# Kernel optimization log

Hardware: AMD Instinct MI355X
Metric: run time of the kernel (lower is better)

Reference implementation:

```python
import jax, jax.numpy as jnp
import numpy as np

N_SLOTS = 16
AGG_THRESHOLD = 0.5
EPS_NORM = 1e-12   # torch F.normalize eps
EPS_AGG = 1e-8


def _l2_normalize(x, axis=-1):
    n = jnp.linalg.norm(x, axis=axis, keepdims=True)
    return x / jnp.maximum(n, EPS_NORM)


def setup_inputs() -> dict:
    key = jax.random.key(0)
    B, N, D = 64, 1024, 768
    features = jax.random.normal(key, (B, N, D), dtype=jnp.float32)
    return {"features": features, "batch_size": B}


def reference(features, batch_size):
    # Greedy slot initialization, saliency_mode='norm', aggregate=True.
    B, N, D = features.shape
    features_norm = _l2_normalize(features, axis=-1)          # [B,N,D]
    saliency = jnp.linalg.norm(features, axis=-1)             # [B,N]

    def step(mask, _):
        # mask: [B,N] multiplicative suppression state
        masked_saliency = saliency * mask
        idx = jnp.argmax(masked_saliency, axis=-1)            # [B]
        selected = jnp.take_along_axis(
            features, idx[:, None, None], axis=1)[:, 0]       # [B,D]
        selected_norm = _l2_normalize(selected, axis=-1)      # [B,D]
        similarity = jnp.einsum('bnd,bd->bn', features_norm, selected_norm)
        # aggregate=True path
        agg_w = jnp.clip(similarity * mask, 0.0, None)
        agg_w = agg_w * (similarity > AGG_THRESHOLD).astype(features.dtype)
        agg_w = agg_w / (jnp.sum(agg_w, axis=-1, keepdims=True) + EPS_AGG)
        slot = jnp.einsum('bn,bnd->bd', agg_w, features)      # [B,D]
        new_mask = mask * (1.0 - jnp.clip(similarity, 0.0, 1.0))
        return new_mask, slot

    init_mask = jnp.ones((B, N), dtype=features.dtype)
    _, slots = jax.lax.scan(step, init_mask, None, length=N_SLOTS)
    return jnp.transpose(slots, (1, 0, 2))                    # [B, n_slots, D]
```

## Files before the change

kernel.cpp:

```cpp
#include <hip/hip_runtime.h>
#include <hip/hip_fp16.h>
#include <math.h>

#define B_      64
#define N_      1024
#define D_      768
#define T_      16
#define SLABS   32
#define ROWS_PB 32
#define ROWS_PW 8
#define THR     256
#define CPL     24
#define NTILE   36
#define WFG     8
#define WFTHR   192

typedef _Float16 half8 __attribute__((ext_vector_type(8)));
typedef float    f32x4 __attribute__((ext_vector_type(4)));

__device__ __forceinline__ float wave_sum(float v) {
    #pragma unroll
    for (int off = 32; off; off >>= 1) v += __shfl_xor(v, off);
    return v;
}
__device__ __forceinline__ float half_sum(float v) {
    #pragma unroll
    for (int off = 16; off; off >>= 1) v += __shfl_xor(v, off);
    return v;
}
__device__ __forceinline__ unsigned pack2(float a, float b) {
    __half2 h = __float22half2_rn(make_float2(a, b));
    return *(unsigned*)&h;
}
__device__ __forceinline__ void unpack8(uint4 u, float* f) {
    __half2 h; float2 q;
    h = *(__half2*)&u.x; q = __half22float2(h); f[0] = q.x; f[1] = q.y;
    h = *(__half2*)&u.y; q = __half22float2(h); f[2] = q.x; f[3] = q.y;
    h = *(__half2*)&u.z; q = __half22float2(h); f[4] = q.x; f[5] = q.y;
    h = *(__half2*)&u.w; q = __half22float2(h); f[6] = q.x; f[7] = q.y;
}

__device__ __forceinline__ void gload_lds16(const void* g, void* l) {
    __builtin_amdgcn_global_load_lds(
        (__attribute__((address_space(1))) void*)(g),
        (__attribute__((address_space(3))) void*)(l), 16, 0, 0);
}

__global__ __launch_bounds__(THR)
void k_sal16v(const float* __restrict__ feat, ushort* __restrict__ f16,
              float* __restrict__ sal, float* __restrict__ rsal,
              float* __restrict__ mask, float* __restrict__ argv,
              float* __restrict__ args, int* __restrict__ argi) {
    const int blk = blockIdx.x, b = blk >> 5, g = blk & 31;
    const int tid = threadIdx.x, wave = tid >> 6, lane = tid & 63;
    const int h = lane >> 5, s = lane & 31;
    __shared__ float s_sal[ROWS_PB];

    const size_t row0 = (size_t)b * N_ + (size_t)g * ROWS_PB;
    const int r0 = wave * ROWS_PW;

    #pragma unroll
    for (int rp = 0; rp < ROWS_PW / 2; ++rp) {
        const int r = r0 + rp * 2 + h;
        const float4* fp4 = (const float4*)(feat + (row0 + r) * D_ + s * CPL);
        float4 a0 = fp4[0], a1 = fp4[1], a2 = fp4[2], a3 = fp4[3], a4 = fp4[4], a5 = fp4[5];
        uint4 w0, w1, w2;
        w0.x = pack2(a0.x, a0.y); w0.y = pack2(a0.z, a0.w);
        w0.z = pack2(a1.x, a1.y); w0.w = pack2(a1.z, a1.w);
        w1.x = pack2(a2.x, a2.y); w1.y = pack2(a2.z, a2.w);
        w1.z = pack2(a3.x, a3.y); w1.w = pack2(a3.z, a3.w);
        w2.x = pack2(a4.x, a4.y); w2.y = pack2(a4.z, a4.w);
        w2.z = pack2(a5.x, a5.y); w2.w = pack2(a5.z, a5.w);
        uint4* wp = (uint4*)(f16 + (row0 + r) * D_ + s * CPL);
        wp[0] = w0; wp[1] = w1; wp[2] = w2;

        float ss = a0.x*a0.x + a0.y*a0.y + a0.z*a0.z + a0.w*a0.w
                 + a1.x*a1.x + a1.y*a1.y + a1.z*a1.z + a1.w*a1.w
                 + a2.x*a2.x + a2.y*a2.y + a2.z*a2.z + a2.w*a2.w
                 + a3.x*a3.x + a3.y*a3.y + a3.z*a3.z + a3.w*a3.w
                 + a4.x*a4.x + a4.y*a4.y + a4.z*a4.z + a4.w*a4.w
                 + a5.x*a5.x + a5.y*a5.y + a5.z*a5.z + a5.w*a5.w;
        ss = half_sum(ss);
        if (s == 0) s_sal[r] = sqrtf(ss);
    }
    __syncthreads();

    const int rg = b * N_ + g * ROWS_PB;
    if (tid < ROWS_PB) {
        float n = s_sal[tid];
        sal[rg + tid]  = n;
        rsal[rg + tid] = 1.0f / fmaxf(n, 1e-12f);
        mask[rg + tid] = 1.0f;
    }
    if (wave == 0) {
        float v  = (lane < ROWS_PB) ? s_sal[lane] : -INFINITY;
        float sv = v;
        int   i  = (lane < ROWS_PB) ? (g * ROWS_PB + lane) : 0x7fffffff;
        #pragma unroll
        for (int off = 32; off; off >>= 1) {
            float ov = __shfl_xor(v, off);
            float osv = __shfl_xor(sv, off);
            int   oi = __shfl_xor(i, off);
            if (ov > v || (ov == v && oi < i)) { v = ov; sv = osv; i = oi; }
        }
        if (lane == 0) { argv[b*SLABS+g] = v; args[b*SLABS+g] = sv; argi[b*SLABS+g] = i; }
    }
}

__global__ __launch_bounds__(THR)
void k_gram(const ushort* __restrict__ f16, float* __restrict__ G) {
    const int bid = blockIdx.x;
    const int xcd = bid & 7, slot = bid >> 3;
    const int batch = xcd + 8 * (slot / NTILE);
    int u = slot % NTILE;
    int trow = 0, cnt = 8;
    while (u >= cnt) { u -= cnt; --cnt; ++trow; }
    const int tcol = trow + u;
    const bool diag = (trow == tcol);

    const int tid = threadIdx.x, wave = tid >> 6, lane = tid & 63;
    const int wr = wave >> 1, wc = wave & 1;

    __shared__ __align__(16) ushort lA[128 * 64];
    __shared__ __align__(16) ushort lB[128 * 64];

    const ushort* Fb = f16 + (size_t)batch * N_ * D_;
    const int row0 = trow * 128, col0 = tcol * 128;

    f32x4 acc[4][4];
    #pragma unroll
    for (int i = 0; i < 4; ++i)
        #pragma unroll
        for (int j = 0; j < 4; ++j)
            acc[i][j] = (f32x4){0.f, 0.f, 0.f, 0.f};

    const ushort* lBr = diag ? lA : lB;

    for (int k0 = 0; k0 < D_; k0 += 64) {
        #pragma unroll
        for (int i = 0; i < 4; ++i) {
            const int d  = i * THR + tid;
            const int r  = d >> 3;
            const int kc = (d & 7) ^ (r & 7);
            gload_lds16(Fb + (size_t)(row0 + r) * D_ + k0 + kc * 8, lA + (size_t)d * 8);
            if (!diag)
                gload_lds16(Fb + (size_t)(col0 + r) * D_ + k0 + kc * 8, lB + (size_t)d * 8);
        }
        __syncthreads();

        #pragma unroll
        for (int ks = 0; ks < 2; ++ks) {
            half8 af[4], bf[4];
            #pragma unroll
            for (int fr = 0; fr < 4; ++fr) {
                const int rl = wr * 64 + fr * 16 + (lane & 15);
                const int kch = ks * 4 + (lane >> 4);
                af[fr] = *(const half8*)(lA + rl * 64 + ((kch ^ (rl & 7)) * 8));
            }
            #pragma unroll
            for (int fc = 0; fc < 4; ++fc) {
                const int cl = wc * 64 + fc * 16 + (lane & 15);
                const int kch = ks * 4 + (lane >> 4);
                bf[fc] = *(const half8*)(lBr + cl * 64 + ((kch ^ (cl & 7)) * 8));
            }
            #pragma unroll
            for (int fr = 0; fr < 4; ++fr)
                #pragma unroll
                for (int fc = 0; fc < 4; ++fc)
                    acc[fr][fc] = __builtin_amdgcn_mfma_f32_16x16x32_f16(
                        af[fr], bf[fc], acc[fr][fc], 0, 0, 0);
        }
        __syncthreads();
    }

    float* Gb = G + ((size_t)batch << 20);
    #pragma unroll
    for (int fr = 0; fr < 4; ++fr) {
        #pragma unroll
        for (int fc = 0; fc < 4; ++fc) {
            const int rbase = row0 + wr * 64 + fr * 16 + (lane >> 4) * 4;
            const int c     = col0 + wc * 64 + fc * 16 + (lane & 15);
            #pragma unroll
            for (int q = 0; q < 4; ++q)
                Gb[(size_t)(rbase + q) * N_ + c] = acc[fr][fc][q];
        }
    }
}

__global__ __launch_bounds__(1024)
void k_slots(const float* __restrict__ G, const float* __restrict__ sal,
             const float* __restrict__ rsal, float* __restrict__ wbuf,
             float* __restrict__ wsum) {
    const int b = blockIdx.x, tid = threadIdx.x, wave = tid >> 6, lane = tid & 63;

    __shared__ float s_sal[N_], s_rsal[N_], s_mask[N_], s_msal[N_];
    __shared__ float s_av[16], s_wv[16];
    __shared__ int   s_ai[16];
    __shared__ int   s_idx;
    __shared__ float s_rsidx;

    {
        const int n = tid;
        float sv = sal[b * N_ + n];
        s_sal[n]  = sv;
        s_rsal[n] = rsal[b * N_ + n];
        s_mask[n] = 1.0f;
        s_msal[n] = sv;
    }
    __syncthreads();

    const float* Gb = G + ((size_t)b << 20);

    for (int t = 0; t < T_; ++t) {
        {
            float v = s_msal[tid]; int i = tid;
            #pragma unroll
            for (int off = 32; off; off >>= 1) {
                float ov = __shfl_xor(v, off);
                int   oi = __shfl_xor(i, off);
                if (ov > v || (ov == v && oi < i)) { v = ov; i = oi; }
            }
            if (lane == 0) { s_av[wave] = v; s_ai[wave] = i; }
        }
        __syncthreads();
        if (tid == 0) {
            float v = s_av[0]; int i = s_ai[0];
            #pragma unroll
            for (int w = 1; w < 16; ++w) {
                float ov = s_av[w]; int oi = s_ai[w];
                if (ov > v || (ov == v && oi < i)) { v = ov; i = oi; }
            }
            s_idx = i;
            s_rsidx = s_rsal[i];
        }
        __syncthreads();

        const int idx = s_idx;
        const float rsi = s_rsidx;

        const int n = tid;
        float gv  = (n >= idx) ? Gb[(size_t)idx * N_ + n]
                               : Gb[(size_t)n * N_ + idx];
        float sim = gv * s_rsal[n] * rsi;
        float m   = s_mask[n];
        float w   = (sim > 0.5f) ? (sim * m) : 0.f;
        float nm  = m * (1.0f - fminf(fmaxf(sim, 0.f), 1.f));
        s_mask[n] = nm;
        s_msal[n] = s_sal[n] * nm;
        wbuf[((size_t)(b * T_ + t)) * N_ + n] = w;
        float wloc = wave_sum(w);
        if (lane == 0) s_wv[wave] = wloc;
        __syncthreads();
        if (tid == 0) {
            float acc = 0.f;
            #pragma unroll
            for (int w2 = 0; w2 < 16; ++w2) acc += s_wv[w2];
            wsum[b * T_ + t] = acc;
        }
        __syncthreads();
    }
}

__global__ __launch_bounds__(WFTHR)
void k_wf(const ushort* __restrict__ f16, const float* __restrict__ wbuf,
          float* __restrict__ part) {
    const int bid = blockIdx.x, b = bid >> 3, rg = bid & 7;
    const int tid = threadIdx.x;
    const int RPG = N_ / WFG;

    __shared__ float s_w[T_ * (N_ / WFG)];

    for (int idx = tid; idx < T_ * RPG; idx += WFTHR) {
        const int t = idx >> 7, r = idx & 127;
        s_w[idx] = wbuf[((size_t)(b * T_ + t)) * N_ + rg * RPG + r];
    }
    __syncthreads();

    float acc[T_][4];
    #pragma unroll
    for (int t = 0; t < T_; ++t) {
        acc[t][0] = 0.f; acc[t][1] = 0.f; acc[t][2] = 0.f; acc[t][3] = 0.f;
    }

    const ushort* Fb = f16 + (size_t)b * N_ * D_;
    for (int r = 0; r < RPG; ++r) {
        const uint2 u = *(const uint2*)(Fb + (size_t)(rg * RPG + r) * D_ + tid * 4);
        __half2 h0 = *(__half2*)&u.x; float2 q0 = __half22float2(h0);
        __half2 h1 = *(__half2*)&u.y; float2 q1 = __half22float2(h1);
        const float f0 = q0.x, f1 = q0.y, f2 = q1.x, f3 = q1.y;
        const float* wr = s_w + r;
        #pragma unroll
        for (int t = 0; t < T_; ++t) {
            const float w = wr[t << 7];
            acc[t][0] = fmaf(w, f0, acc[t][0]);
            acc[t][1] = fmaf(w, f1, acc[t][1]);
            acc[t][2] = fmaf(w, f2, acc[t][2]);
            acc[t][3] = fmaf(w, f3, acc[t][3]);
        }
    }

    float* pb = part + (((size_t)(b * WFG + rg)) * T_) * D_;
    #pragma unroll
    for (int t = 0; t < T_; ++t) {
        float4 v; v.x = acc[t][0]; v.y = acc[t][1]; v.z = acc[t][2]; v.w = acc[t][3];
        *(float4*)(pb + (size_t)t * D_ + tid * 4) = v;
    }
}

__global__ __launch_bounds__(THR)
void k_red(const float* __restrict__ part, const float* __restrict__ wsum,
           float* __restrict__ out) {
    const int bid = blockIdx.x, b = bid >> 4, t = bid & 15;
    const int tid = threadIdx.x;
    const float den = wsum[b * T_ + t] + 1e-8f;
    #pragma unroll
    for (int j = 0; j < 3; ++j) {
        const int c = tid + j * 256;
        float s = 0.f;
        #pragma unroll
        for (int rg = 0; rg < WFG; ++rg)
            s += part[(((size_t)(b * WFG + rg)) * T_ + t) * D_ + c];
        out[((size_t)(b * T_ + t)) * D_ + c] = s / den;
    }
}

__global__ __launch_bounds__(THR)
void k_fusedv(const ushort* __restrict__ f16, const float* __restrict__ sel,
              const float* __restrict__ sal, const float* __restrict__ rsal,
              float* __restrict__ mask, float* __restrict__ num,
              float* __restrict__ wsum, float* __restrict__ argv,
              float* __restrict__ args, int* __restrict__ argi) {
    const int blk = blockIdx.x, b = blk >> 5, g = blk & 31;
    const int tid = threadIdx.x, wave = tid >> 6, lane = tid & 63;
    const int h = lane >> 5, s = lane & 31;
    __shared__ __align__(16) float s_red[4 * D_];
    __shared__ float s_wsumW[4];
    __shared__ float s_msal[ROWS_PB];
    __shared__ float s_salL[ROWS_PB];
    const size_t row0 = (size_t)b * N_ + (size_t)g * ROWS_PB;
    const int rbase = b * N_ + g * ROWS_PB;
    const int r0 = wave * ROWS_PW;
    float se[CPL];
    {
        const float4* sp = (const float4*)(sel + (size_t)b * D_ + s * CPL);
        #pragma unroll
        for (int q = 0; q < 6; ++q) {
            float4 v = sp[q];
            se[q*4+0] = v.x; se[q*4+1] = v.y; se[q*4+2] = v.z; se[q*4+3] = v.w;
        }
    }
    float acc[CPL];
    #pragma unroll
    for (int i = 0; i < CPL; ++i) acc[i] = 0.f;
    float wsl = 0.f;
    #pragma unroll
    for (int rp = 0; rp < ROWS_PW / 2; ++rp) {
        const int r = r0 + rp * 2 + h;
        const uint4* dp = (const uint4*)(f16 + (row0 + r) * D_ + s * CPL);
        uint4 u0 = dp[0], u1 = dp[1], u2 = dp[2];
        float f[CPL];
        unpack8(u0, f); unpack8(u1, f + 8); unpack8(u2, f + 16);
        float dot = 0.f;
        #pragma unroll
        for (int i = 0; i < CPL; ++i) dot = fmaf(f[i], se[i], dot);
        dot = half_sum(dot);
        float rs  = rsal[rbase + r];
        float sv  = sal[rbase + r];
        float m   = mask[rbase + r];
        float sim = dot * rs;
        float wr  = (sim > 0.5f) ? (sim * m) : 0.f;
        float nm  = m * (1.0f - fminf(fmaxf(sim, 0.f), 1.f));
        if (s == 0) { mask[rbase + r] = nm; s_msal[r] = sv * nm; s_salL[r] = sv; }
        wsl += wr;
        #pragma unroll
        for (int i = 0; i < CPL; ++i) acc[i] = fmaf(wr, f[i], acc[i]);
    }
    wsl += __shfl_xor(wsl, 32);
    #pragma unroll
    for (int i = 0; i < CPL; ++i) acc[i] += __shfl_xor(acc[i], 32);
    if (h == 0) {
        float4* rw = (float4*)(s_red + wave * D_ + s * CPL);
        #pragma unroll
        for (int q = 0; q < 6; ++q) {
            float4 v;
            v.x = acc[q*4+0]; v.y = acc[q*4+1]; v.z = acc[q*4+2]; v.w = acc[q*4+3];
            rw[q] = v;
        }
    }
    if (lane == 0) s_wsumW[wave] = wsl;
    __syncthreads();
    #pragma unroll
    for (int it = 0; it < 3; ++it) {
        const int c = it * THR + tid;
        float sm = s_red[c] + s_red[D_ + c] + s_red[2*D_ + c] + s_red[3*D_ + c];
        num[((size_t)b * SLABS + g) * D_ + c] = sm;
    }
    if (tid == 0)
        wsum[b*SLABS+g] = s_wsumW[0] + s_wsumW[1] + s_wsumW[2] + s_wsumW[3];
    if (wave == 0) {
        float v  = (lane < ROWS_PB) ? s_msal[lane] : -INFINITY;
        float sv = (lane < ROWS_PB) ? s_salL[lane] : 0.f;
        int   i  = (lane < ROWS_PB) ? (g * ROWS_PB + lane) : 0x7fffffff;
        #pragma unroll
        for (int off = 32; off; off >>= 1) {
            float ov = __shfl_xor(v, off);
            float osv = __shfl_xor(sv, off);
            int   oi = __shfl_xor(i, off);
            if (ov > v || (ov == v && oi < i)) { v = ov; sv = osv; i = oi; }
        }
        if (lane == 0) { argv[b*SLABS+g] = v; args[b*SLABS+g] = sv; argi[b*SLABS+g] = i; }
    }
}

__global__ __launch_bounds__(192)
void k_out(const float* __restrict__ feat, const float* __restrict__ num,
           const float* __restrict__ wsumA, const float* __restrict__ argv,
           const float* __restrict__ args, const int* __restrict__ argi,
           float* __restrict__ sel, float* __restrict__ out, int t) {
    const int b = blockIdx.x >> 2, q = blockIdx.x & 3;
    const int tid = threadIdx.x, lane = tid & 63;
    __shared__ float s_rsel;
    __shared__ int   s_idx;
    __shared__ float s_ws;
    if (tid < 64) {
        float v  = (lane < SLABS) ? argv[b*SLABS + lane] : -INFINITY;
        float sv = (lane < SLABS) ? args[b*SLABS + lane] : 0.f;
        int   i  = (lane < SLABS) ? argi[b*SLABS + lane] : 0x7fffffff;
        float w  = (lane < SLABS) ? wsumA[b*SLABS + lane] : 0.f;
        #pragma unroll
        for (int off = 32; off; off >>= 1) {
            float ov = __shfl_xor(v, off);
            float osv = __shfl_xor(sv, off);
            int   oi = __shfl_xor(i, off);
            w += __shfl_xor(w, off);
            if (ov > v || (ov == v && oi < i)) { v = ov; sv = osv; i = oi; }
        }
        if (lane == 0) { s_idx = i; s_rsel = 1.0f / fmaxf(sv, 1e-12f); s_ws = w; }
    }
    __syncthreads();
    const int c = q * 192 + tid;
    if (t >= 0) {
        float sm = 0.f;
        #pragma unroll 8
        for (int g = 0; g < SLABS; ++g)
            sm += num[((size_t)b * SLABS + g) * D_ + c];
        out[((size_t)b * T_ + t) * D_ + c] = sm / (s_ws + 1e-8f);
    }
    sel[(size_t)b * D_ + c] = feat[((size_t)b * N_ + s_idx) * D_ + c] * s_rsel;
}

extern "C" void kernel_launch(void* const* d_in, const int* in_sizes, int n_in,
                              void* d_out, int out_size, void* d_ws, size_t ws_size,
                              hipStream_t stream) {
    const float* feat = (const float*)d_in[0];
    float* out = (float*)d_out;
    (void)in_sizes; (void)n_in; (void)out_size;

    const size_t n_sal  = (size_t)B_ * N_;
    const size_t n_arg  = (size_t)B_ * SLABS;
    const size_t n_sel  = (size_t)B_ * D_;
    const size_t n_num  = (size_t)B_ * SLABS * D_;
    const size_t n_f16  = (size_t)B_ * N_ * D_;
    const size_t n_G    = (size_t)B_ * N_ * N_;
    const size_t n_wbuf = (size_t)B_ * T_ * N_;
    const size_t n_part = (size_t)B_ * WFG * T_ * D_;

    const size_t f16_bytes = (n_f16 * sizeof(ushort) + 255) & ~(size_t)255;

    const size_t need_gram = f16_bytes
        + (n_G + n_wbuf + n_part + 3*n_sal + (size_t)B_*T_ + 3*n_arg) * sizeof(float) + 4096;
    const size_t need_mk = f16_bytes
        + (3*n_sal + 4*n_arg + n_sel + n_num) * sizeof(float) + 1024;

    if (ws_size >= need_gram) {
        char* base = (char*)d_ws;
        ushort* f16 = (ushort*)base;
        float* p = (float*)(base + f16_bytes);
        float* G     = p;        p += n_G;
        float* wbuf  = p;        p += n_wbuf;
        float* part  = p;        p += n_part;
        float* sal   = p;        p += n_sal;
        float* rsal  = p;        p += n_sal;
        float* mask  = p;        p += n_sal;
        float* wsum  = p;        p += (size_t)B_ * T_;
        float* argvD = p;        p += n_arg;
        float* argsD = p;        p += n_arg;
        int*   argiD = (int*)p;  p += n_arg;

        k_sal16v<<<B_*SLABS, THR, 0, stream>>>(feat, f16, sal, rsal, mask,
                                               argvD, argsD, argiD);
        k_gram<<<B_*NTILE, THR, 0, stream>>>(f16, G);
        k_slots<<<B_, 1024, 0, stream>>>(G, sal, rsal, wbuf, wsum);
        k_wf<<<B_*WFG, WFTHR, 0, stream>>>(f16, wbuf, part);
        k_red<<<B_*T_, THR, 0, stream>>>(part, wsum, out);
        return;
    }

    if (ws_size >= need_mk) {
        char* base = (char*)d_ws;
        ushort* f16 = (ushort*)base;
        float* p = (float*)(base + f16_bytes);
        float* sal  = p;            p += n_sal;
        float* rsal = p;            p += n_sal;
        float* mask = p;            p += n_sal;
        float* argv = p;            p += n_arg;
        float* args = p;            p += n_arg;
        int*   argi = (int*)p;      p += n_arg;
        float* wsum = p;            p += n_arg;
        float* sel  = p;            p += n_sel;
        float* num  = p;            p += n_num;

        k_sal16v<<<B_*SLABS, THR, 0, stream>>>(feat, f16, sal, rsal, mask, argv, args, argi);
        k_out<<<B_*4, 192, 0, stream>>>(feat, num, wsum, argv, args, argi, sel, out, -1);
        for (int t = 0; t < T_; ++t) {
            k_fusedv<<<B_*SLABS, THR, 0, stream>>>(f16, sel, sal, rsal, mask,
                                                   num, wsum, argv, args, argi);
            k_out<<<B_*4, 192, 0, stream>>>(feat, num, wsum, argv, args, argi, sel, out, t);
        }
        return;
    }
}
```

Baseline: 254.7 us.

## Run greedy slot selection in a single wavefront and move weight sums downstream

The per-batch slot-selection kernel shrinks from 1024 threads to one 64-lane wavefront. Each lane keeps 16 rows of saliency and mask state in registers, so the block-wide barriers and shared-memory argmax and sum reductions are gone. The weight-sum normalisation now comes from per-row-group partial sums in the weighted-feature kernel, which the final reduce kernel adds up. The trade is that each lane now issues 16 serial gram-matrix gathers per step with less memory parallelism, and only 64 wavefronts cover the whole GPU.

```diff
diff --git a/kernel.cpp b/kernel.cpp
--- a/kernel.cpp
+++ b/kernel.cpp
@@ -187,83 +187,56 @@
     }
 }
 
-__global__ __launch_bounds__(1024)
+__global__ __launch_bounds__(64)
 void k_slots(const float* __restrict__ G, const float* __restrict__ sal,
-             const float* __restrict__ rsal, float* __restrict__ wbuf,
-             float* __restrict__ wsum) {
-    const int b = blockIdx.x, tid = threadIdx.x, wave = tid >> 6, lane = tid & 63;
-
-    __shared__ float s_sal[N_], s_rsal[N_], s_mask[N_], s_msal[N_];
-    __shared__ float s_av[16], s_wv[16];
-    __shared__ int   s_ai[16];
-    __shared__ int   s_idx;
-    __shared__ float s_rsidx;
-
-    {
-        const int n = tid;
-        float sv = sal[b * N_ + n];
-        s_sal[n]  = sv;
-        s_rsal[n] = rsal[b * N_ + n];
-        s_mask[n] = 1.0f;
-        s_msal[n] = sv;
-    }
-    __syncthreads();
-
+             const float* __restrict__ rsal, float* __restrict__ wbuf) {
+    const int b = blockIdx.x, lane = threadIdx.x;
     const float* Gb = G + ((size_t)b << 20);
 
+    float lsal[16], lrsal[16], lmask[16], lmsal[16];
+    #pragma unroll
+    for (int k = 0; k < 16; ++k) {
+        const int n = lane + (k << 6);
+        lsal[k]  = sal[b * N_ + n];
+        lrsal[k] = rsal[b * N_ + n];
+        lmask[k] = 1.0f;
+        lmsal[k] = lsal[k];
+    }
+
     for (int t = 0; t < T_; ++t) {
-        {
-            float v = s_msal[tid]; int i = tid;
-            #pragma unroll
-            for (int off = 32; off; off >>= 1) {
-                float ov = __shfl_xor(v, off);
-                int   oi = __shfl_xor(i, off);
-                if (ov > v || (ov == v && oi < i)) { v = ov; i = oi; }
-            }
-            if (lane == 0) { s_av[wave] = v; s_ai[wave] = i; }
-        }
-        __syncthreads();
-        if (tid == 0) {
-            float v = s_av[0]; int i = s_ai[0];
-            #pragma unroll
-            for (int w = 1; w < 16; ++w) {
-                float ov = s_av[w]; int oi = s_ai[w];
-                if (ov > v || (ov == v && oi < i)) { v = ov; i = oi; }
-            }
-            s_idx = i;
-            s_rsidx = s_rsal[i];
-        }
-        __syncthreads();
-
-        const int idx = s_idx;
-        const float rsi = s_rsidx;
-
-        const int n = tid;
-        float gv  = (n >= idx) ? Gb[(size_t)idx * N_ + n]
-                               : Gb[(size_t)n * N_ + idx];
-        float sim = gv * s_rsal[n] * rsi;
-        float m   = s_mask[n];
-        float w   = (sim > 0.5f) ? (sim * m) : 0.f;
-        float nm  = m * (1.0f - fminf(fmaxf(sim, 0.f), 1.f));
-        s_mask[n] = nm;
-        s_msal[n] = s_sal[n] * nm;
-        wbuf[((size_t)(b * T_ + t)) * N_ + n] = w;
-        float wloc = wave_sum(w);
-        if (lane == 0) s_wv[wave] = wloc;
-        __syncthreads();
-        if (tid == 0) {
-            float acc = 0.f;
-            #pragma unroll
-            for (int w2 = 0; w2 < 16; ++w2) acc += s_wv[w2];
-            wsum[b * T_ + t] = acc;
-        }
-        __syncthreads();
+        float v = lmsal[0]; int i = lane;
+        #pragma unroll
+        for (int k = 1; k < 16; ++k) {
+            if (lmsal[k] > v) { v = lmsal[k]; i = lane + (k << 6); }
+        }
+        #pragma unroll
+        for (int off = 32; off; off >>= 1) {
+            float ov = __shfl_xor(v, off);
+            int   oi = __shfl_xor(i, off);
+            if (ov > v || (ov == v && oi < i)) { v = ov; i = oi; }
+        }
+        const int idx = i;
+        const float rsi = rsal[b * N_ + idx];
+
+        #pragma unroll
+        for (int k = 0; k < 16; ++k) {
+            const int n = lane + (k << 6);
+            float gv  = (n >= idx) ? Gb[(size_t)idx * N_ + n]
+                                   : Gb[(size_t)n * N_ + idx];
+            float sim = gv * lrsal[k] * rsi;
+            float m   = lmask[k];
+            float w   = (sim > 0.5f) ? (sim * m) : 0.f;
+            float nm  = m * (1.0f - fminf(fmaxf(sim, 0.f), 1.f));
+            lmask[k] = nm;
+            lmsal[k] = lsal[k] * nm;
+            wbuf[((size_t)(b * T_ + t)) * N_ + n] = w;
+        }
     }
 }
 
 __global__ __launch_bounds__(WFTHR)
 void k_wf(const ushort* __restrict__ f16, const float* __restrict__ wbuf,
-          float* __restrict__ part) {
+          float* __restrict__ part, float* __restrict__ wsp) {
     const int bid = blockIdx.x, b = bid >> 3, rg = bid & 7;
     const int tid = threadIdx.x;
     const int RPG = N_ / WFG;
@@ -275,6 +248,13 @@
         s_w[idx] = wbuf[((size_t)(b * T_ + t)) * N_ + rg * RPG + r];
     }
     __syncthreads();
+
+    if (tid < T_) {
+        float s = 0.f;
+        #pragma unroll 8
+        for (int r = 0; r < RPG; ++r) s += s_w[tid * RPG + r];
+        wsp[((size_t)(b * WFG + rg)) * T_ + tid] = s;
+    }
 
     float acc[T_][4];
     #pragma unroll
@@ -308,11 +288,15 @@
 }
 
 __global__ __launch_bounds__(THR)
-void k_red(const float* __restrict__ part, const float* __restrict__ wsum,
+void k_red(const float* __restrict__ part, const float* __restrict__ wsp,
            float* __restrict__ out) {
     const int bid = blockIdx.x, b = bid >> 4, t = bid & 15;
     const int tid = threadIdx.x;
-    const float den = wsum[b * T_ + t] + 1e-8f;
+    float den = 0.f;
+    #pragma unroll
+    for (int rg = 0; rg < WFG; ++rg)
+        den += wsp[((size_t)(b * WFG + rg)) * T_ + t];
+    den += 1e-8f;
     #pragma unroll
     for (int j = 0; j < 3; ++j) {
         const int c = tid + j * 256;
@@ -464,11 +448,12 @@
     const size_t n_G    = (size_t)B_ * N_ * N_;
     const size_t n_wbuf = (size_t)B_ * T_ * N_;
     const size_t n_part = (size_t)B_ * WFG * T_ * D_;
+    const size_t n_wsp  = (size_t)B_ * WFG * T_;
 
     const size_t f16_bytes = (n_f16 * sizeof(ushort) + 255) & ~(size_t)255;
 
     const size_t need_gram = f16_bytes
-        + (n_G + n_wbuf + n_part + 3*n_sal + (size_t)B_*T_ + 3*n_arg) * sizeof(float) + 4096;
+        + (n_G + n_wbuf + n_part + n_wsp + 3*n_sal + 3*n_arg) * sizeof(float) + 4096;
     const size_t need_mk = f16_bytes
         + (3*n_sal + 4*n_arg + n_sel + n_num) * sizeof(float) + 1024;
 
@@ -479,10 +464,10 @@
         float* G     = p;        p += n_G;
         float* wbuf  = p;        p += n_wbuf;
         float* part  = p;        p += n_part;
+        float* wsp   = p;        p += n_wsp;
         float* sal   = p;        p += n_sal;
         float* rsal  = p;        p += n_sal;
         float* mask  = p;        p += n_sal;
-        float* wsum  = p;        p += (size_t)B_ * T_;
         float* argvD = p;        p += n_arg;
         float* argsD = p;        p += n_arg;
         int*   argiD = (int*)p;  p += n_arg;
@@ -490,9 +475,9 @@
         k_sal16v<<<B_*SLABS, THR, 0, stream>>>(feat, f16, sal, rsal, mask,
                                                argvD, argsD, argiD);
         k_gram<<<B_*NTILE, THR, 0, stream>>>(f16, G);
-        k_slots<<<B_, 1024, 0, stream>>>(G, sal, rsal, wbuf, wsum);
-        k_wf<<<B_*WFG, WFTHR, 0, stream>>>(f16, wbuf, part);
-        k_red<<<B_*T_, THR, 0, stream>>>(part, wsum, out);
+        k_slots<<<B_, 64, 0, stream>>>(G, sal, rsal, wbuf);
+        k_wf<<<B_*WFG, WFTHR, 0, stream>>>(f16, wbuf, part, wsp);
+        k_red<<<B_*T_, THR, 0, stream>>>(part, wsp, out);
         return;
     }
 
```

New measurement: 237.4 us (median of 2 runs). 1.07x faster.
